# Kernel optimization log

Measured on AMD Instinct MI355X. Metric: run time of the kernel, lower is better.

Reference implementation:

```python
import jax, jax.numpy as jnp
from jax import lax
import numpy as np

B, P, C = 16, 21824, 2          # batch, num_priors, num_classes
KCAND = 1024                    # candidate cap for jittable NMS
TOP_K = 750
CONF_THRESH = 0.3
IOU_THRESH = 0.01
VAR = (0.1, 0.2)
IMG_SCALE = 1024.0


def setup_inputs() -> dict:
    key = jax.random.key(0)
    k1, k2, k3 = jax.random.split(key, 3)
    return {
        "boxes_logits": jax.random.normal(k1, (B, P, 4), dtype=jnp.float32),
        "cls_logits": jax.random.normal(k2, (B, P, C), dtype=jnp.float32),
        "priors": jax.random.uniform(k3, (P, 4), dtype=jnp.float32),
    }


def decode(loc, priors):
    # priors are (cx, cy, w, h); loc are SSD-style offsets
    xy = priors[..., :2] + loc[..., :2] * VAR[0] * priors[..., 2:]
    wh = priors[..., 2:] * jnp.exp(loc[..., 2:] * VAR[1])
    x1y1 = xy - wh * 0.5
    x2y2 = x1y1 + wh
    return jnp.concatenate([x1y1, x2y2], axis=-1) * IMG_SCALE


def iou_matrix(b):
    # b: [K,4] in x1y1x2y2; torchvision-style IoU (areas unclamped, inter clamped)
    area = (b[:, 2] - b[:, 0]) * (b[:, 3] - b[:, 1])
    lt = jnp.maximum(b[:, None, :2], b[None, :, :2])
    rb = jnp.minimum(b[:, None, 2:], b[None, :, 2:])
    wh = jnp.clip(rb - lt, 0.0)
    inter = wh[..., 0] * wh[..., 1]
    union = area[:, None] + area[None, :] - inter
    return inter / jnp.maximum(union, 1e-9)


def greedy_nms(iou, valid, thresh):
    # boxes assumed sorted by descending score; returns keep mask [K]
    K = iou.shape[0]
    iou = jnp.where(jnp.eye(K, dtype=bool), 0.0, iou)  # ignore self-overlap

    def step(suppressed, i):
        keep_i = jnp.logical_and(~suppressed[i], valid[i])
        suppressed = jnp.logical_or(suppressed, keep_i & (iou[i] > thresh))
        return suppressed, keep_i

    _, keep = lax.scan(step, jnp.zeros(K, dtype=bool), jnp.arange(K))
    return keep


def _detect_one(boxes, scores_all):
    # boxes [P,4], scores_all [P,C]
    scores = scores_all[:, 1:].reshape(-1)                        # drop background
    labels = jnp.broadcast_to(jnp.arange(1, C), (P, C - 1)).reshape(-1)
    bx = jnp.broadcast_to(boxes[:, None, :], (P, C - 1, 4)).reshape(-1, 4)

    masked = jnp.where(scores > CONF_THRESH, scores, -1.0)
    top_scores, idx = lax.top_k(masked, KCAND)                    # score-sorted candidates
    cb = bx[idx]                                                  # [K,4]
    cl = labels[idx]                                              # [K]
    valid = top_scores > CONF_THRESH

    # batched_nms: offset boxes per class so classes never overlap
    max_c = jnp.max(jnp.where(valid[:, None], cb, 0.0))
    off = cl.astype(cb.dtype)[:, None] * (max_c + 1.0)
    keep = greedy_nms(iou_matrix(cb + off), valid, IOU_THRESH)

    kept_scores = jnp.where(keep, top_scores, -1.0)
    final_s, kidx = lax.top_k(kept_scores, TOP_K)                 # keep[:top_k] in score order
    mask = keep[kidx]
    out_boxes = jnp.where(mask[:, None], cb[kidx], 0.0)
    out_scores = jnp.where(mask, final_s, 0.0)
    out_labels = jnp.where(mask, cl[kidx], 0)
    return out_boxes, out_scores, out_labels, mask


def reference(boxes_logits, cls_logits, priors):
    scores_logits = jax.nn.softmax(cls_logits, axis=2)            # [B,P,C]
    boxes = decode(boxes_logits, priors)                          # [B,P,4]
    pred_boxes, pred_scores, pred_labels, mask = jax.vmap(_detect_one)(boxes, scores_logits)
    return pred_boxes, pred_scores, pred_labels, mask
```

## Files before the change

kernel.cpp:

```cpp
#include <hip/hip_runtime.h>

typedef unsigned long long u64;
typedef unsigned int u32;

#define KC 1024
#define TOPK 750
#define CONF 0.3f
#define IOU_T 0.01f
#define WINB 0x2F80u
#define NW 128
#define CCAP 2048

__device__ __forceinline__ u64 score_key(const float* __restrict__ c2, u32 p) {
    float a0 = c2[0], a1 = c2[1];
    float m  = fmaxf(a0, a1);
    float e0 = expf(a0 - m), e1 = expf(a1 - m);
    float s  = e1 / (e0 + e1);
    float ms = s > CONF ? s : -1.0f;
    u32 u = __float_as_uint(ms);
    u32 mapped = (u & 0x80000000u) ? ~u : (u | 0x80000000u);
    return ((u64)mapped << 32) | (u32)(~p);
}

__global__ __launch_bounds__(1024) void k_hist(const float* __restrict__ cls,
                                               u32* __restrict__ hist, int P) {
    __shared__ u32 lh[NW];
    int t = threadIdx.x;
    if (t < NW) lh[t] = 0;
    __syncthreads();
    int p = blockIdx.x * 1024 + t;
    int b = blockIdx.y;
    if (p < P) {
        u64 k = score_key(cls + ((size_t)b * P + p) * 2, (u32)p);
        u32 wbin = (u32)(k >> 50) - WINB;
        if (wbin < (u32)NW) atomicAdd(&lh[wbin], 1u);
    }
    __syncthreads();
    if (t < NW) { u32 c = lh[t]; if (c) atomicAdd(&hist[(size_t)b * NW + t], c); }
}

__global__ __launch_bounds__(256) void k_compact(const float* __restrict__ cls,
        const u32* __restrict__ hist, u32* __restrict__ sufx, u32* __restrict__ tot,
        u32* __restrict__ bfill, u64* __restrict__ cbuf2, int P) {
    int b = blockIdx.y, t = threadIdx.x;
    __shared__ u32 sh[NW], sa[NW], sb_[NW];
    __shared__ int sh_cut;
    if (t == 0) sh_cut = 0;
    if (t < NW) { u32 h = hist[(size_t)b * NW + t]; sh[t] = h; sa[t] = h; }
    __syncthreads();
    u32 *src = sa, *dst = sb_;
    for (int d = 1; d < NW; d <<= 1) {
        if (t < NW) dst[t] = src[t] + ((t + d < NW) ? src[t + d] : 0u);
        __syncthreads();
        u32* tmp = src; src = dst; dst = tmp;
    }
    if (t < NW && src[t] >= KC) atomicMax(&sh_cut, t);
    __syncthreads();
    int cutw = sh_cut;
    if (blockIdx.x == 0) {
        if (t < NW) sufx[(size_t)b * NW + t] = src[t] - sh[t];
        if (t == 0) tot[b] = src[cutw];
    }
    int p = blockIdx.x * 256 + t;
    if (p < P) {
        u64 k = score_key(cls + ((size_t)b * P + p) * 2, (u32)p);
        u32 wbin = (u32)(k >> 50) - WINB;
        if (wbin < (u32)NW && (int)wbin >= cutw) {
            u32 pos = (src[wbin] - sh[wbin]) + atomicAdd(&bfill[(size_t)b * NW + wbin], 1u);
            if (pos < CCAP) cbuf2[(size_t)b * CCAP + pos] = k;
        }
    }
}

__global__ void k_rankdec(const u64* __restrict__ cbuf2, const u32* __restrict__ hist,
                          const u32* __restrict__ sufx, const u32* __restrict__ tot,
                          u64* __restrict__ csorted, float* __restrict__ cboxes,
                          const float* __restrict__ bl, const float* __restrict__ priors,
                          int P) {
    int b = blockIdx.y;
    u32 s = blockIdx.x * 64 + threadIdx.x;
    u32 T = tot[b]; if (T > CCAP) T = CCAP;
    if (s >= T) return;
    const u64* cb = cbuf2 + (size_t)b * CCAP;
    u64 key = cb[s];
    u32 w = (u32)(key >> 50) - WINB;
    u32 seg0 = sufx[(size_t)b * NW + w];
    u32 segN = seg0 + hist[(size_t)b * NW + w];
    if (segN > T) segN = T;
    u32 cnt = 0;
    for (u32 j = seg0; j < segN; ++j) cnt += (cb[j] > key) ? 1u : 0u;
    u32 r = seg0 + cnt;
    if (r >= KC) return;
    csorted[(size_t)b * KC + r] = key;

    u32 p = ~(u32)(key & 0xffffffffull);
    const float* pr4 = priors + (size_t)p * 4;
    const float* lc  = bl + ((size_t)b * P + p) * 4;
    float pcx = pr4[0], pcy = pr4[1], pw = pr4[2], ph = pr4[3];
    float lx = lc[0], ly = lc[1], lw = lc[2], lh = lc[3];
    float cx = pcx + lx * 0.1f * pw;
    float cy = pcy + ly * 0.1f * ph;
    float ww = pw * expf(lw * 0.2f);
    float hh = ph * expf(lh * 0.2f);
    float t1x = cx - ww * 0.5f;
    float t1y = cy - hh * 0.5f;
    float4 bx;
    bx.x = t1x * 1024.0f;
    bx.y = t1y * 1024.0f;
    bx.z = (t1x + ww) * 1024.0f;
    bx.w = (t1y + hh) * 1024.0f;
    *reinterpret_cast<float4*>(cboxes + ((size_t)b * KC + r) * 4) = bx;
}

__global__ __launch_bounds__(1024) void k_iou(const u64* __restrict__ csorted,
        const float* __restrict__ cboxes, u64* __restrict__ rows) {
    int b = blockIdx.y, tid = threadIdx.x;
    __shared__ float sx1[KC], sy1[KC], sx2[KC], sy2[KC], sar[KC];
    __shared__ float smax[KC];
    u64 key = csorted[(size_t)b * KC + tid];
    bool valid = (key != 0ull);
    float4 bx = reinterpret_cast<const float4*>(cboxes + (size_t)b * KC * 4)[tid];
    smax[tid] = valid ? fmaxf(fmaxf(bx.x, bx.y), fmaxf(bx.z, bx.w)) : 0.0f;
    __syncthreads();
    for (int st = 512; st > 0; st >>= 1) {
        if (tid < st) smax[tid] = fmaxf(smax[tid], smax[tid + st]);
        __syncthreads();
    }
    float off = smax[0] + 1.0f;
    float xs1 = bx.x + off, ys1 = bx.y + off, xs2 = bx.z + off, ys2 = bx.w + off;
    sx1[tid] = xs1; sy1[tid] = ys1; sx2[tid] = xs2; sy2[tid] = ys2;
    sar[tid] = (xs2 - xs1) * (ys2 - ys1);
    __syncthreads();

    int w = tid >> 6, lane = tid & 63;
    u64* rbb = rows + (size_t)b * KC * 16;
    #pragma unroll
    for (int rr = 0; rr < 4; ++rr) {
        int r = blockIdx.x * 64 + w * 4 + rr;
        float rx1 = sx1[r], ry1 = sy1[r], rx2 = sx2[r], ry2 = sy2[r], rar = sar[r];
        u64* rb = rbb + (size_t)r * 16;
        #pragma unroll 4
        for (int c = 0; c < 16; ++c) {
            int col = c * 64 + lane;
            float ltx = fmaxf(rx1, sx1[col]), lty = fmaxf(ry1, sy1[col]);
            float rbx = fminf(rx2, sx2[col]), rby = fminf(ry2, sy2[col]);
            float w2 = fmaxf(rbx - ltx, 0.0f), h2 = fmaxf(rby - lty, 0.0f);
            float inter = w2 * h2;
            float uni = rar + sar[col] - inter;
            float iou = inter / fmaxf(uni, 1e-9f);
            bool pred = (iou > IOU_T) && (col != r);
            u64 m = __ballot(pred);
            if (lane == 0) rb[c] = m;
        }
    }
}

__global__ __launch_bounds__(1024) void k_scan(const u64* __restrict__ csorted,
        const u64* __restrict__ rows, const float* __restrict__ cboxes,
        float* __restrict__ out, int B) {
    int b = blockIdx.x, tid = threadIdx.x;
    __shared__ u64 vw[16], keepw[16];
    u64 key = csorted[(size_t)b * KC + tid];
    bool valid = (key != 0ull);
    u32 mapped = (u32)(key >> 32);
    u32 fb = (mapped & 0x80000000u) ? (mapped & 0x7fffffffu) : ~mapped;
    float score = __uint_as_float(fb);
    u64 bal = __ballot(valid);
    if ((tid & 63) == 0) vw[tid >> 6] = bal;
    __syncthreads();

    if (tid < 16) {
        int lane = tid;
        u64 supp = ~vw[lane];
        u64 kw = 0;
        const u64* rb = rows + (size_t)b * KC * 16;
        for (int w = 0; w < 16; ++w) {
            u64 sw = __shfl(supp, w);
            u64 rem = ~sw;
            while (rem) {
                int bit = __ffsll((long long)rem) - 1;
                int i = w * 64 + bit;
                supp |= rb[(size_t)i * 16 + lane];
                if (lane == w) kw |= 1ull << bit;
                sw = __shfl(supp, w);
                u64 above = (bit == 63) ? 0ull : (~0ull << (bit + 1));
                rem = ~sw & above;
            }
        }
        keepw[lane] = kw;
    }
    __syncthreads();

    int wq = tid >> 6, bq = tid & 63;
    u64 myw = keepw[wq];
    bool kept = (myw >> bq) & 1ull;
    int rank = 0, nk = 0;
    #pragma unroll
    for (int w2 = 0; w2 < 16; ++w2) {
        int pc = __popcll(keepw[w2]);
        nk += pc;
        if (w2 < wq) rank += pc;
    }
    rank += __popcll(myw & ((1ull << bq) - 1ull));

    float* ob  = out;
    float* osc = out + (size_t)B * TOPK * 4;
    float* olb = osc + (size_t)B * TOPK;
    float* omk = olb + (size_t)B * TOPK;

    if (kept && rank < TOPK) {
        size_t o = (size_t)b * TOPK + rank;
        float4 bx = reinterpret_cast<const float4*>(cboxes)[(size_t)b * KC + tid];
        *reinterpret_cast<float4*>(ob + o * 4) = bx;
        osc[o] = score;
        olb[o] = 1.0f;
        omk[o] = 1.0f;
    }
    int zstart = nk < TOPK ? nk : TOPK;
    if (tid >= zstart && tid < TOPK) {
        size_t o = (size_t)b * TOPK + tid;
        float4 z; z.x = z.y = z.z = z.w = 0.0f;
        *reinterpret_cast<float4*>(ob + o * 4) = z;
        osc[o] = 0.0f;
        olb[o] = 0.0f;
        omk[o] = 0.0f;
    }
}

extern "C" void kernel_launch(void* const* d_in, const int* in_sizes, int n_in,
                              void* d_out, int out_size, void* d_ws, size_t ws_size,
                              hipStream_t stream) {
    const float* boxes_logits = (const float*)d_in[0];
    const float* cls_logits   = (const float*)d_in[1];
    const float* priors       = (const float*)d_in[2];
    int P = in_sizes[2] / 4;
    int B = in_sizes[0] / (P * 4);
    float* out = (float*)d_out;
    char* wsb = (char*)d_ws;

    size_t HIST_B  = (size_t)B * NW * sizeof(u32);
    size_t BFILL_B = (size_t)B * NW * sizeof(u32);
    size_t CSORT_B = (size_t)B * KC * sizeof(u64);
    size_t SUFX_B  = (size_t)B * NW * sizeof(u32);
    size_t TOT_B   = 256;
    size_t CBUF2_B = (size_t)B * CCAP * sizeof(u64);
    size_t CBOX_B  = (size_t)B * KC * 4 * sizeof(float);
    u32* hist    = (u32*)wsb;
    u32* bfill   = (u32*)(wsb + HIST_B);
    u64* csorted = (u64*)(wsb + HIST_B + BFILL_B);
    u32* sufx    = (u32*)(wsb + HIST_B + BFILL_B + CSORT_B);
    u32* tot     = (u32*)(wsb + HIST_B + BFILL_B + CSORT_B + SUFX_B);
    u64* cbuf2   = (u64*)(wsb + HIST_B + BFILL_B + CSORT_B + SUFX_B + TOT_B);
    float* cboxes= (float*)(wsb + HIST_B + BFILL_B + CSORT_B + SUFX_B + TOT_B + CBUF2_B);
    u64* rows    = (u64*)(wsb + HIST_B + BFILL_B + CSORT_B + SUFX_B + TOT_B + CBUF2_B + CBOX_B);

    hipMemsetAsync(wsb, 0, HIST_B + BFILL_B + CSORT_B, stream);

    hipLaunchKernelGGL(k_hist,    dim3((P + 1023) / 1024, B), dim3(1024), 0, stream,
                       cls_logits, hist, P);
    hipLaunchKernelGGL(k_compact, dim3((P + 255) / 256, B),   dim3(256),  0, stream,
                       cls_logits, hist, sufx, tot, bfill, cbuf2, P);
    hipLaunchKernelGGL(k_rankdec, dim3(CCAP / 64, B),         dim3(64),   0, stream,
                       cbuf2, hist, sufx, tot, csorted, cboxes, boxes_logits, priors, P);
    hipLaunchKernelGGL(k_iou,     dim3(KC / 64, B),           dim3(1024), 0, stream,
                       csorted, cboxes, rows);
    hipLaunchKernelGGL(k_scan,    dim3(B),                    dim3(1024), 0, stream,
                       csorted, rows, cboxes, out, B);
}
```

Before: 154.0 us.

## Fuse histogram, compaction, rank sort and decode into one per-batch kernel

Replaces the k_hist, k_compact and k_rankdec kernels and the workspace memset with a single k_sel kernel that runs one 1024-thread block per batch. Histogram, suffix scan, compaction and rank sort all happen in shared memory. Box decode and the class-offset max reduction are also moved in, with the offset passed to k_iou through a small buffer. This removes several launches, the memset and global-memory round trips. In exchange each batch is handled by one block that scans all priors twice, so only 16 blocks run across the GPU during selection.

```diff
diff --git a/kernel.cpp b/kernel.cpp
--- a/kernel.cpp
+++ b/kernel.cpp
@@ -22,111 +22,106 @@
     return ((u64)mapped << 32) | (u32)(~p);
 }
 
-__global__ __launch_bounds__(1024) void k_hist(const float* __restrict__ cls,
-                                               u32* __restrict__ hist, int P) {
-    __shared__ u32 lh[NW];
-    int t = threadIdx.x;
-    if (t < NW) lh[t] = 0;
-    __syncthreads();
-    int p = blockIdx.x * 1024 + t;
-    int b = blockIdx.y;
-    if (p < P) {
-        u64 k = score_key(cls + ((size_t)b * P + p) * 2, (u32)p);
+__global__ __launch_bounds__(1024) void k_sel(const float* __restrict__ cls,
+        const float* __restrict__ bl, const float* __restrict__ priors,
+        u64* __restrict__ csorted, float* __restrict__ cboxes,
+        float* __restrict__ coffs, int P) {
+    int b = blockIdx.x, tid = threadIdx.x;
+    __shared__ u32 sh[NW], sa[NW], sb_[NW], sufx[NW], bfill[NW];
+    __shared__ int sh_cut;
+    __shared__ u32 sh_T;
+    __shared__ u64 keys2[CCAP];
+    __shared__ u64 ksorted[KC];
+    __shared__ float smax[KC];
+
+    if (tid < NW) { sh[tid] = 0; bfill[tid] = 0; }
+    if (tid == 0) sh_cut = 0;
+    ksorted[tid] = 0;
+    __syncthreads();
+
+    const float* cb2 = cls + (size_t)b * P * 2;
+    for (int i = tid; i < P; i += 1024) {
+        u64 k = score_key(cb2 + (size_t)i * 2, (u32)i);
         u32 wbin = (u32)(k >> 50) - WINB;
-        if (wbin < (u32)NW) atomicAdd(&lh[wbin], 1u);
-    }
-    __syncthreads();
-    if (t < NW) { u32 c = lh[t]; if (c) atomicAdd(&hist[(size_t)b * NW + t], c); }
-}
-
-__global__ __launch_bounds__(256) void k_compact(const float* __restrict__ cls,
-        const u32* __restrict__ hist, u32* __restrict__ sufx, u32* __restrict__ tot,
-        u32* __restrict__ bfill, u64* __restrict__ cbuf2, int P) {
-    int b = blockIdx.y, t = threadIdx.x;
-    __shared__ u32 sh[NW], sa[NW], sb_[NW];
-    __shared__ int sh_cut;
-    if (t == 0) sh_cut = 0;
-    if (t < NW) { u32 h = hist[(size_t)b * NW + t]; sh[t] = h; sa[t] = h; }
+        if (wbin < (u32)NW) atomicAdd(&sh[wbin], 1u);
+    }
+    __syncthreads();
+    if (tid < NW) sa[tid] = sh[tid];
     __syncthreads();
     u32 *src = sa, *dst = sb_;
     for (int d = 1; d < NW; d <<= 1) {
-        if (t < NW) dst[t] = src[t] + ((t + d < NW) ? src[t + d] : 0u);
+        if (tid < NW) dst[tid] = src[tid] + ((tid + d < NW) ? src[tid + d] : 0u);
         __syncthreads();
         u32* tmp = src; src = dst; dst = tmp;
     }
-    if (t < NW && src[t] >= KC) atomicMax(&sh_cut, t);
+    if (tid < NW && src[tid] >= KC) atomicMax(&sh_cut, tid);
     __syncthreads();
     int cutw = sh_cut;
-    if (blockIdx.x == 0) {
-        if (t < NW) sufx[(size_t)b * NW + t] = src[t] - sh[t];
-        if (t == 0) tot[b] = src[cutw];
-    }
-    int p = blockIdx.x * 256 + t;
-    if (p < P) {
-        u64 k = score_key(cls + ((size_t)b * P + p) * 2, (u32)p);
+    if (tid < NW) sufx[tid] = src[tid] - sh[tid];
+    if (tid == 0) sh_T = src[cutw];
+    __syncthreads();
+
+    for (int i = tid; i < P; i += 1024) {
+        u64 k = score_key(cb2 + (size_t)i * 2, (u32)i);
         u32 wbin = (u32)(k >> 50) - WINB;
         if (wbin < (u32)NW && (int)wbin >= cutw) {
-            u32 pos = (src[wbin] - sh[wbin]) + atomicAdd(&bfill[(size_t)b * NW + wbin], 1u);
-            if (pos < CCAP) cbuf2[(size_t)b * CCAP + pos] = k;
+            u32 pos = sufx[wbin] + atomicAdd(&bfill[wbin], 1u);
+            if (pos < CCAP) keys2[pos] = k;
         }
     }
-}
-
-__global__ void k_rankdec(const u64* __restrict__ cbuf2, const u32* __restrict__ hist,
-                          const u32* __restrict__ sufx, const u32* __restrict__ tot,
-                          u64* __restrict__ csorted, float* __restrict__ cboxes,
-                          const float* __restrict__ bl, const float* __restrict__ priors,
-                          int P) {
-    int b = blockIdx.y;
-    u32 s = blockIdx.x * 64 + threadIdx.x;
-    u32 T = tot[b]; if (T > CCAP) T = CCAP;
-    if (s >= T) return;
-    const u64* cb = cbuf2 + (size_t)b * CCAP;
-    u64 key = cb[s];
-    u32 w = (u32)(key >> 50) - WINB;
-    u32 seg0 = sufx[(size_t)b * NW + w];
-    u32 segN = seg0 + hist[(size_t)b * NW + w];
-    if (segN > T) segN = T;
-    u32 cnt = 0;
-    for (u32 j = seg0; j < segN; ++j) cnt += (cb[j] > key) ? 1u : 0u;
-    u32 r = seg0 + cnt;
-    if (r >= KC) return;
-    csorted[(size_t)b * KC + r] = key;
-
-    u32 p = ~(u32)(key & 0xffffffffull);
-    const float* pr4 = priors + (size_t)p * 4;
-    const float* lc  = bl + ((size_t)b * P + p) * 4;
-    float pcx = pr4[0], pcy = pr4[1], pw = pr4[2], ph = pr4[3];
-    float lx = lc[0], ly = lc[1], lw = lc[2], lh = lc[3];
-    float cx = pcx + lx * 0.1f * pw;
-    float cy = pcy + ly * 0.1f * ph;
-    float ww = pw * expf(lw * 0.2f);
-    float hh = ph * expf(lh * 0.2f);
-    float t1x = cx - ww * 0.5f;
-    float t1y = cy - hh * 0.5f;
-    float4 bx;
-    bx.x = t1x * 1024.0f;
-    bx.y = t1y * 1024.0f;
-    bx.z = (t1x + ww) * 1024.0f;
-    bx.w = (t1y + hh) * 1024.0f;
-    *reinterpret_cast<float4*>(cboxes + ((size_t)b * KC + r) * 4) = bx;
-}
-
-__global__ __launch_bounds__(1024) void k_iou(const u64* __restrict__ csorted,
-        const float* __restrict__ cboxes, u64* __restrict__ rows) {
-    int b = blockIdx.y, tid = threadIdx.x;
-    __shared__ float sx1[KC], sy1[KC], sx2[KC], sy2[KC], sar[KC];
-    __shared__ float smax[KC];
-    u64 key = csorted[(size_t)b * KC + tid];
+    __syncthreads();
+
+    u32 T = sh_T; if (T > CCAP) T = CCAP;
+    for (int c = tid; c < (int)T; c += 1024) {
+        u64 key = keys2[c];
+        u32 w = (u32)(key >> 50) - WINB;
+        u32 seg0 = sufx[w];
+        u32 segN = seg0 + sh[w];
+        if (segN > T) segN = T;
+        u32 cnt = 0;
+        for (u32 j = seg0; j < segN; ++j) cnt += (keys2[j] > key) ? 1u : 0u;
+        u32 r = seg0 + cnt;
+        if (r < KC) ksorted[r] = key;
+    }
+    __syncthreads();
+
+    u64 key = ksorted[tid];
     bool valid = (key != 0ull);
-    float4 bx = reinterpret_cast<const float4*>(cboxes + (size_t)b * KC * 4)[tid];
+    float4 bx; bx.x = bx.y = bx.z = bx.w = 0.0f;
+    if (valid) {
+        u32 p = ~(u32)(key & 0xffffffffull);
+        const float* pr4 = priors + (size_t)p * 4;
+        const float* lc  = bl + ((size_t)b * P + p) * 4;
+        float pcx = pr4[0], pcy = pr4[1], pw = pr4[2], ph = pr4[3];
+        float lx = lc[0], ly = lc[1], lw = lc[2], lh = lc[3];
+        float cx = pcx + lx * 0.1f * pw;
+        float cy = pcy + ly * 0.1f * ph;
+        float ww = pw * expf(lw * 0.2f);
+        float hh = ph * expf(lh * 0.2f);
+        float t1x = cx - ww * 0.5f;
+        float t1y = cy - hh * 0.5f;
+        bx.x = t1x * 1024.0f;
+        bx.y = t1y * 1024.0f;
+        bx.z = (t1x + ww) * 1024.0f;
+        bx.w = (t1y + hh) * 1024.0f;
+    }
+    csorted[(size_t)b * KC + tid] = key;
+    reinterpret_cast<float4*>(cboxes)[(size_t)b * KC + tid] = bx;
     smax[tid] = valid ? fmaxf(fmaxf(bx.x, bx.y), fmaxf(bx.z, bx.w)) : 0.0f;
     __syncthreads();
     for (int st = 512; st > 0; st >>= 1) {
         if (tid < st) smax[tid] = fmaxf(smax[tid], smax[tid + st]);
         __syncthreads();
     }
-    float off = smax[0] + 1.0f;
+    if (tid == 0) coffs[b] = smax[0] + 1.0f;
+}
+
+__global__ __launch_bounds__(1024) void k_iou(const float* __restrict__ cboxes,
+        const float* __restrict__ coffs, u64* __restrict__ rows) {
+    int b = blockIdx.y, tid = threadIdx.x;
+    __shared__ float sx1[KC], sy1[KC], sx2[KC], sy2[KC], sar[KC];
+    float off = coffs[b];
+    float4 bx = reinterpret_cast<const float4*>(cboxes)[(size_t)b * KC + tid];
     float xs1 = bx.x + off, ys1 = bx.y + off, xs2 = bx.z + off, ys2 = bx.w + off;
     sx1[tid] = xs1; sy1[tid] = ys1; sx2[tid] = xs2; sy2[tid] = ys2;
     sar[tid] = (xs2 - xs1) * (ys2 - ys1);
@@ -238,32 +233,18 @@
     float* out = (float*)d_out;
     char* wsb = (char*)d_ws;
 
-    size_t HIST_B  = (size_t)B * NW * sizeof(u32);
-    size_t BFILL_B = (size_t)B * NW * sizeof(u32);
     size_t CSORT_B = (size_t)B * KC * sizeof(u64);
-    size_t SUFX_B  = (size_t)B * NW * sizeof(u32);
-    size_t TOT_B   = 256;
-    size_t CBUF2_B = (size_t)B * CCAP * sizeof(u64);
     size_t CBOX_B  = (size_t)B * KC * 4 * sizeof(float);
-    u32* hist    = (u32*)wsb;
-    u32* bfill   = (u32*)(wsb + HIST_B);
-    u64* csorted = (u64*)(wsb + HIST_B + BFILL_B);
-    u32* sufx    = (u32*)(wsb + HIST_B + BFILL_B + CSORT_B);
-    u32* tot     = (u32*)(wsb + HIST_B + BFILL_B + CSORT_B + SUFX_B);
-    u64* cbuf2   = (u64*)(wsb + HIST_B + BFILL_B + CSORT_B + SUFX_B + TOT_B);
-    float* cboxes= (float*)(wsb + HIST_B + BFILL_B + CSORT_B + SUFX_B + TOT_B + CBUF2_B);
-    u64* rows    = (u64*)(wsb + HIST_B + BFILL_B + CSORT_B + SUFX_B + TOT_B + CBUF2_B + CBOX_B);
-
-    hipMemsetAsync(wsb, 0, HIST_B + BFILL_B + CSORT_B, stream);
-
-    hipLaunchKernelGGL(k_hist,    dim3((P + 1023) / 1024, B), dim3(1024), 0, stream,
-                       cls_logits, hist, P);
-    hipLaunchKernelGGL(k_compact, dim3((P + 255) / 256, B),   dim3(256),  0, stream,
-                       cls_logits, hist, sufx, tot, bfill, cbuf2, P);
-    hipLaunchKernelGGL(k_rankdec, dim3(CCAP / 64, B),         dim3(64),   0, stream,
-                       cbuf2, hist, sufx, tot, csorted, cboxes, boxes_logits, priors, P);
-    hipLaunchKernelGGL(k_iou,     dim3(KC / 64, B),           dim3(1024), 0, stream,
-                       csorted, cboxes, rows);
-    hipLaunchKernelGGL(k_scan,    dim3(B),                    dim3(1024), 0, stream,
+    size_t COFF_B  = 256;
+    u64*   csorted = (u64*)wsb;
+    float* cboxes  = (float*)(wsb + CSORT_B);
+    float* coffs   = (float*)(wsb + CSORT_B + CBOX_B);
+    u64*   rows    = (u64*)(wsb + CSORT_B + CBOX_B + COFF_B);
+
+    hipLaunchKernelGGL(k_sel,  dim3(B),         dim3(1024), 0, stream,
+                       cls_logits, boxes_logits, priors, csorted, cboxes, coffs, P);
+    hipLaunchKernelGGL(k_iou,  dim3(KC / 64, B), dim3(1024), 0, stream,
+                       cboxes, coffs, rows);
+    hipLaunchKernelGGL(k_scan, dim3(B),         dim3(1024), 0, stream,
                        csorted, rows, cboxes, out, B);
 }
```

New measurement: 145.9 us. -5.2%, faster.
